# Optimization experiments

Measured on AMD Instinct MI355X. Metric: run time of the kernel, lower is better.

## Reference

```python
import jax, jax.numpy as jnp
import numpy as np

B, S, D, H = 2, 2048, 1024, 16
HD = D // H  # head_dim = 64


def setup_inputs() -> dict:
    key = jax.random.key(0)
    k1, k2, k3 = jax.random.split(key, 3)
    x = jax.random.normal(k1, (B, S, D), dtype=jnp.float32)
    W_attn = jax.random.normal(k2, (3 * D, D), dtype=jnp.float32) * (D ** -0.5)
    W_proj = jax.random.normal(k3, (D, D), dtype=jnp.float32) * (D ** -0.5)
    b_proj = jnp.zeros((D,), dtype=jnp.float32)
    return {"x": x, "W_attn": W_attn, "W_proj": W_proj, "b_proj": b_proj}


def reference(x, W_attn, W_proj, b_proj):
    b, s, d = x.shape
    h, hd = H, d // H
    # fused QKV projection (torch Linear: x @ W^T), then split
    qkv = jnp.einsum('bsd,ed->bse', x, W_attn)  # [B,S,3D]
    q, k, v = jnp.split(qkv, 3, axis=-1)
    # [B,S,D] -> [B,H,S,hd]
    q = q.reshape(b, s, h, hd).transpose(0, 2, 1, 3)
    k = k.reshape(b, s, h, hd).transpose(0, 2, 1, 3)
    v = v.reshape(b, s, h, hd).transpose(0, 2, 1, 3)
    # manual softmax attention (no causal mask in the non-flash branch)
    att = jnp.einsum('bhqd,bhkd->bhqk', q, k) * (1.0 / jnp.sqrt(jnp.float32(hd)))
    att = jax.nn.softmax(att, axis=-1)  # attn_dropout is identity in eval
    y = jnp.einsum('bhqk,bhkd->bhqd', att, v)
    y = y.transpose(0, 2, 1, 3).reshape(b, s, d)
    y = jnp.einsum('bsd,ed->bse', y, W_proj) + b_proj  # resid_dropout identity
    return y, att
```

## Files before the change

### kernel.cpp

```cpp
#include <hip/hip_runtime.h>

typedef _Float16 f16;
typedef f16 f16x4 __attribute__((ext_vector_type(4)));
typedef f16 f16x8 __attribute__((ext_vector_type(8)));
typedef float f32x4 __attribute__((ext_vector_type(4)));
typedef unsigned int u32;
typedef unsigned long long u64;

#define DEV static __device__ __forceinline__

#define S_ 2048
#define D_ 1024

#define S_WAITV(n) asm volatile("s_waitcnt vmcnt(" #n ") lgkmcnt(0)" ::: "memory")

DEV int swz64(int row, int chunk) { return row * 64 + (((chunk ^ row) & 7) << 3); }

DEV void gload16(const void* g, void* l) {
    __builtin_amdgcn_global_load_lds((const __attribute__((address_space(1))) u32*)g,
                                     (__attribute__((address_space(3))) u32*)l, 16, 0, 0);
}
DEV float exp2_fast(float x) { float r; asm("v_exp_f32 %0, %1" : "=v"(r) : "v"(x)); return r; }

__global__ void convert_f16(const float* __restrict__ x, const float* __restrict__ wa,
                            const float* __restrict__ wp,
                            f16* __restrict__ xb, f16* __restrict__ wab, f16* __restrict__ wpb) {
    u32 t = blockIdx.x * blockDim.x + threadIdx.x;
    u32 base = t * 8u;
    const float* src; f16* dst; u32 off;
    if (base < 4194304u)      { src = x;  dst = xb;  off = base; }
    else if (base < 7340032u) { src = wa; dst = wab; off = base - 4194304u; }
    else                      { src = wp; dst = wpb; off = base - 7340032u; }
    float4 a = *(const float4*)(src + off);
    float4 b = *(const float4*)(src + off + 4);
    f16x8 v;
    v[0] = (f16)a.x; v[1] = (f16)a.y; v[2] = (f16)a.z; v[3] = (f16)a.w;
    v[4] = (f16)b.x; v[5] = (f16)b.y; v[6] = (f16)b.z; v[7] = (f16)b.w;
    *(f16x8*)(dst + off) = v;
}

template <int EPI>
__global__ __launch_bounds__(256) void gemm_bt(
    const f16* __restrict__ A, const f16* __restrict__ Bt, int K,
    f16* __restrict__ oQ, f16* __restrict__ oK, f16* __restrict__ oV,
    float* __restrict__ oY, const float* __restrict__ bias) {
    __shared__ f16 smem[8704];
    f16* As = smem;
    f16* Bs = smem + 4096;
    const int tid = threadIdx.x;
    const int lane = tid & 63;
    const int la = lane & 15, lg = lane >> 4;
    const int wv = tid >> 6;
    const int wr = (wv >> 1) << 6, wc = (wv & 1) << 6;
    const int r0 = blockIdx.x << 7, c0 = blockIdx.y << 7;

    const f32x4 VZ = {0.f, 0.f, 0.f, 0.f};
    f32x4 acc[4][4];
#pragma unroll
    for (int m = 0; m < 4; ++m)
#pragma unroll
        for (int n = 0; n < 4; ++n) acc[m][n] = VZ;

    const int srow = tid >> 2, scol = (tid & 3) << 3;
    const f16* Ag = A + (u64)(r0 + srow) * K + scol;
    const f16* Bg = Bt + (u64)(c0 + srow) * K + scol;
    const u64 K64 = (u64)K << 6;
    f16* Al = As + wv * 512;
    f16* Bl = Bs + wv * 512;

    for (int k0 = 0; k0 < K; k0 += 32) {
        __syncthreads();
        gload16(Ag + k0, Al);
        gload16(Ag + K64 + k0, Al + 2048);
        gload16(Bg + k0, Bl);
        gload16(Bg + K64 + k0, Bl + 2048);
        __syncthreads();
        f16x8 af[4], bf[4];
#pragma unroll
        for (int m = 0; m < 4; ++m) af[m] = *(const f16x8*)(As + (wr + m * 16 + la) * 32 + lg * 8);
#pragma unroll
        for (int n = 0; n < 4; ++n) bf[n] = *(const f16x8*)(Bs + (wc + n * 16 + la) * 32 + lg * 8);
#pragma unroll
        for (int m = 0; m < 4; ++m)
#pragma unroll
            for (int n = 0; n < 4; ++n)
                acc[m][n] = __builtin_amdgcn_mfma_f32_16x16x32_f16(af[m], bf[n], acc[m][n], 0, 0, 0);
    }

    if (EPI == 0) {
        if (c0 < 2048) {
#pragma unroll
            for (int n = 0; n < 4; ++n) {
                int col = c0 + wc + n * 16 + la;
#pragma unroll
                for (int m = 0; m < 4; ++m) {
#pragma unroll
                    for (int j = 0; j < 4; ++j) {
                        int row = r0 + wr + m * 16 + lg * 4 + j;
                        int b = row >> 11, s = row & 2047;
                        float val = acc[m][n][j];
                        if (col < 1024) {
                            int h = col >> 6, hd = col & 63;
                            oQ[(((u64)(b * 16 + h)) * 2048 + s) * 64 + hd] = (f16)(val * 0.18033688f);
                        } else {
                            int d = col - 1024, h = d >> 6, hd = d & 63;
                            oK[(((u64)(b * 16 + h)) * 2048 + s) * 64 + hd] = (f16)val;
                        }
                    }
                }
            }
        } else {
            const int hbase = (c0 - 2048) >> 6;
            const int b = r0 >> 11, sb = r0 & 2047;
#pragma unroll
            for (int hh = 0; hh < 2; ++hh) {
                __syncthreads();
                if ((wv & 1) == hh) {
#pragma unroll
                    for (int n = 0; n < 4; ++n) {
                        int hd = n * 16 + la;
#pragma unroll
                        for (int m = 0; m < 4; ++m) {
                            int s = wr + m * 16 + lg * 4;
                            int pos = (s & ~31) | (lg << 3) | (((s >> 4) & 1) << 2);
                            f16x4 pk;
                            pk[0] = (f16)acc[m][n][0]; pk[1] = (f16)acc[m][n][1];
                            pk[2] = (f16)acc[m][n][2]; pk[3] = (f16)acc[m][n][3];
                            *(f16x4*)(smem + hd * 136 + pos) = pk;
                        }
                    }
                }
                __syncthreads();
                {
                    int hd = tid >> 2, qtr = tid & 3;
                    f16* dst = oV + (((u64)(b * 16 + hbase + hh)) * 64 + hd) * 2048 + sb + qtr * 32;
#pragma unroll
                    for (int i = 0; i < 4; ++i)
                        *(f16x8*)(dst + i * 8) = *(const f16x8*)(smem + hd * 136 + qtr * 32 + i * 8);
                }
            }
        }
    } else {
#pragma unroll
        for (int n = 0; n < 4; ++n) {
            int col = c0 + wc + n * 16 + la;
            float bv = bias[col];
#pragma unroll
            for (int m = 0; m < 4; ++m)
#pragma unroll
                for (int j = 0; j < 4; ++j) {
                    int row = r0 + wr + m * 16 + lg * 4 + j;
                    oY[(u64)row * 1024 + col] = acc[m][n][j] + bv;
                }
        }
    }
}

__global__ __launch_bounds__(256) void attn_fused(
    const f16* __restrict__ q, const f16* __restrict__ k, const f16* __restrict__ vt,
    float* __restrict__ att, f16* __restrict__ ya) {
    __shared__ f16 smem[5 * 4096];
    f16* qs = smem + 4 * 4096;

    const int tid = threadIdx.x, lane = tid & 63, wv = tid >> 6;
    const int la = lane & 15, lg = lane >> 4;
    const int qt = blockIdx.x, bh = blockIdx.y;
    const f16* qh = q + (u64)bh * (S_ * 64) + qt * (64 * 64);
    const f16* kh = k + (u64)bh * (S_ * 64);
    const f16* vh = vt + (u64)bh * (S_ * 64);

    const int sr0 = wv * 8 + (lane >> 3);
    const int sr1 = sr0 + 32;
    const int sc0 = (((lane & 7) ^ (sr0 & 7)) << 3);
    const int sc1 = (((lane & 7) ^ (sr1 & 7)) << 3);
    const u64 go0 = (u64)sr0 * 64 + sc0, go1 = (u64)sr1 * 64 + sc1;
    const u64 gv0 = (u64)sr0 * 2048 + sc0, gv1 = (u64)sr1 * 2048 + sc1;

    gload16(qh + go0, qs + wv * 512);
    gload16(qh + go1, qs + 2048 + wv * 512);
    gload16(kh + go0, smem + wv * 512);
    gload16(kh + go1, smem + 2048 + wv * 512);
    gload16(kh + 4096 + go0, smem + 4096 + wv * 512);
    gload16(kh + 4096 + go1, smem + 4096 + 2048 + wv * 512);
    S_WAITV(2);
    __builtin_amdgcn_s_barrier();

    f16x8 qf[2];
    qf[0] = *(const f16x8*)(qs + swz64(wv * 16 + la, lg));
    qf[1] = *(const f16x8*)(qs + swz64(wv * 16 + la, 4 + lg));

    const f32x4 VZ = {0.f, 0.f, 0.f, 0.f};
    float psum = 0.f;

    for (int kt = 0; kt < 32; ++kt) {
        if (kt > 0) {
            if (kt < 31) { S_WAITV(2); } else { S_WAITV(0); }
            __builtin_amdgcn_s_barrier();
        }
        if (kt < 30) {
            const f16* kb = kh + (kt + 2) * 4096;
            f16* dst = smem + ((kt + 2) % 3) * 4096;
            gload16(kb + go0, dst + wv * 512);
            gload16(kb + go1, dst + 2048 + wv * 512);
        }
        const f16* kcur = smem + (kt % 3) * 4096;
        f32x4 sc[4] = {VZ, VZ, VZ, VZ};
#pragma unroll
        for (int ch = 0; ch < 2; ++ch)
#pragma unroll
            for (int n = 0; n < 4; ++n) {
                f16x8 kf = *(const f16x8*)(kcur + swz64(n * 16 + la, ch * 4 + lg));
                sc[n] = __builtin_amdgcn_mfma_f32_16x16x32_f16(kf, qf[ch], sc[n], 0, 0, 0);
            }
#pragma unroll
        for (int n = 0; n < 4; ++n)
#pragma unroll
            for (int j = 0; j < 4; ++j) psum += exp2_fast(sc[n][j]);
    }
    S_WAITV(0);
    __builtin_amdgcn_s_barrier();

    psum += __shfl_xor(psum, 16);
    psum += __shfl_xor(psum, 32);
    const float invl = 1.0f / psum;

    gload16(kh + go0, smem + wv * 512);
    gload16(kh + go1, smem + 2048 + wv * 512);
    gload16(vh + gv0, smem + 2 * 4096 + wv * 512);
    gload16(vh + gv1, smem + 2 * 4096 + 2048 + wv * 512);
    S_WAITV(0);
    __builtin_amdgcn_s_barrier();

    f32x4 accy[4] = {VZ, VZ, VZ, VZ};
    float* ab = att + ((u64)bh * S_ + (u64)qt * 64 + wv * 16 + la) * S_ + (lg << 2);
    for (int kt = 0; kt < 32; ++kt) {
        if (kt > 0) {
            S_WAITV(4);
            __builtin_amdgcn_s_barrier();
        }
        if (kt < 31) {
            const f16* kb = kh + (kt + 1) * 4096;
            const f16* vb = vh + (kt + 1) * 64;
            f16* kd = smem + ((kt + 1) & 1) * 4096;
            f16* vd = smem + (2 + ((kt + 1) & 1)) * 4096;
            gload16(kb + go0, kd + wv * 512);
            gload16(kb + go1, kd + 2048 + wv * 512);
            gload16(vb + gv0, vd + wv * 512);
            gload16(vb + gv1, vd + 2048 + wv * 512);
        }
        const f16* kcur = smem + (kt & 1) * 4096;
        const f16* vcur = smem + (2 + (kt & 1)) * 4096;

        f32x4 sc[4] = {VZ, VZ, VZ, VZ};
#pragma unroll
        for (int ch = 0; ch < 2; ++ch)
#pragma unroll
            for (int n = 0; n < 4; ++n) {
                f16x8 kf = *(const f16x8*)(kcur + swz64(n * 16 + la, ch * 4 + lg));
                sc[n] = __builtin_amdgcn_mfma_f32_16x16x32_f16(kf, qf[ch], sc[n], 0, 0, 0);
            }
        f32x4 pp[4];
#pragma unroll
        for (int n = 0; n < 4; ++n) {
#pragma unroll
            for (int j = 0; j < 4; ++j) pp[n][j] = exp2_fast(sc[n][j]) * invl;
            *(f32x4*)(ab + kt * 64 + n * 16) = pp[n];
        }
        f16x8 pa0, pa1;
#pragma unroll
        for (int j = 0; j < 4; ++j) {
            pa0[j] = (f16)pp[0][j]; pa0[j + 4] = (f16)pp[1][j];
            pa1[j] = (f16)pp[2][j]; pa1[j + 4] = (f16)pp[3][j];
        }
#pragma unroll
        for (int n = 0; n < 4; ++n) {
            f16x8 vf0 = *(const f16x8*)(vcur + swz64(n * 16 + la, lg));
            accy[n] = __builtin_amdgcn_mfma_f32_16x16x32_f16(pa0, vf0, accy[n], 0, 0, 0);
            f16x8 vf1 = *(const f16x8*)(vcur + swz64(n * 16 + la, 4 + lg));
            accy[n] = __builtin_amdgcn_mfma_f32_16x16x32_f16(pa1, vf1, accy[n], 0, 0, 0);
        }
    }

    const int b = bh >> 4, h = bh & 15;
    f16* yb = ya + ((u64)b * S_ + qt * 64 + wv * 16) * D_ + h * 64;
#pragma unroll
    for (int n = 0; n < 4; ++n)
#pragma unroll
        for (int j = 0; j < 4; ++j)
            yb[(u64)(lg * 4 + j) * D_ + n * 16 + la] = (f16)accy[n][j];
}

extern "C" void kernel_launch(void* const* d_in, const int* in_sizes, int n_in,
                              void* d_out, int out_size, void* d_ws, size_t ws_size,
                              hipStream_t stream) {
    const float* x  = (const float*)d_in[0];
    const float* wa = (const float*)d_in[1];
    const float* wp = (const float*)d_in[2];
    const float* bp = (const float*)d_in[3];
    float* outY   = (float*)d_out;
    float* outAtt = outY + 4194304ull;

    char* ws = (char*)d_ws;
    f16* xb  = (f16*)(ws + 0);
    f16* wab = (f16*)(ws + 8388608);
    f16* wpb = (f16*)(ws + 14680064);
    f16* qb  = (f16*)(ws + 16777216);
    f16* kb  = (f16*)(ws + 25165824);
    f16* vtb = (f16*)(ws + 33554432);
    f16* yab = (f16*)(ws + 41943040);

    convert_f16<<<4096, 256, 0, stream>>>(x, wa, wp, xb, wab, wpb);
    gemm_bt<0><<<dim3(32, 24), 256, 0, stream>>>(xb, wab, 1024, qb, kb, vtb, nullptr, nullptr);
    attn_fused<<<dim3(32, 32), 256, 0, stream>>>(qb, kb, vtb, outAtt, yab);
    gemm_bt<1><<<dim3(32, 8), 256, 0, stream>>>(yab, wpb, 1024, nullptr, nullptr, nullptr, outY, bp);
}
```

Baseline: 258.7 us.

## Triple-buffer GEMM LDS tiles with async global-to-LDS prefetch two stages ahead

```diff
diff --git a/kernel.cpp b/kernel.cpp
--- a/kernel.cpp
+++ b/kernel.cpp
@@ -44,9 +44,8 @@
     const f16* __restrict__ A, const f16* __restrict__ Bt, int K,
     f16* __restrict__ oQ, f16* __restrict__ oK, f16* __restrict__ oV,
     float* __restrict__ oY, const float* __restrict__ bias) {
-    __shared__ f16 smem[8704];
-    f16* As = smem;
-    f16* Bs = smem + 4096;
+    __shared__ f16 smem[3][8192];
+    f16* sm = &smem[0][0];
     const int tid = threadIdx.x;
     const int lane = tid & 63;
     const int la = lane & 15, lg = lane >> 4;
@@ -65,16 +64,31 @@
     const f16* Ag = A + (u64)(r0 + srow) * K + scol;
     const f16* Bg = Bt + (u64)(c0 + srow) * K + scol;
     const u64 K64 = (u64)K << 6;
-    f16* Al = As + wv * 512;
-    f16* Bl = Bs + wv * 512;
-
-    for (int k0 = 0; k0 < K; k0 += 32) {
-        __syncthreads();
-        gload16(Ag + k0, Al);
-        gload16(Ag + K64 + k0, Al + 2048);
-        gload16(Bg + k0, Bl);
-        gload16(Bg + K64 + k0, Bl + 2048);
-        __syncthreads();
+
+    const int NT = K >> 5;
+#define STAGE(k0, slot)                                              \
+    do {                                                             \
+        f16* Al = smem[slot] + wv * 512;                             \
+        f16* Bl = smem[slot] + 4096 + wv * 512;                      \
+        gload16(Ag + (k0), Al);                                      \
+        gload16(Ag + K64 + (k0), Al + 2048);                         \
+        gload16(Bg + (k0), Bl);                                      \
+        gload16(Bg + K64 + (k0), Bl + 2048);                         \
+    } while (0)
+
+    STAGE(0, 0);
+    STAGE(32, 1);
+    S_WAITV(4);
+    __builtin_amdgcn_s_barrier();
+
+    for (int t = 0; t < NT; ++t) {
+        if (t > 0) {
+            if (t < NT - 1) { S_WAITV(4); } else { S_WAITV(0); }
+            __builtin_amdgcn_s_barrier();
+        }
+        if (t + 2 < NT) STAGE((t + 2) << 5, (t + 2) % 3);
+        const f16* As = smem[t % 3];
+        const f16* Bs = smem[t % 3] + 4096;
         f16x8 af[4], bf[4];
 #pragma unroll
         for (int m = 0; m < 4; ++m) af[m] = *(const f16x8*)(As + (wr + m * 16 + la) * 32 + lg * 8);
@@ -86,6 +100,7 @@
             for (int n = 0; n < 4; ++n)
                 acc[m][n] = __builtin_amdgcn_mfma_f32_16x16x32_f16(af[m], bf[n], acc[m][n], 0, 0, 0);
     }
+#undef STAGE
 
     if (EPI == 0) {
         if (c0 < 2048) {
@@ -126,7 +141,7 @@
                             f16x4 pk;
                             pk[0] = (f16)acc[m][n][0]; pk[1] = (f16)acc[m][n][1];
                             pk[2] = (f16)acc[m][n][2]; pk[3] = (f16)acc[m][n][3];
-                            *(f16x4*)(smem + hd * 136 + pos) = pk;
+                            *(f16x4*)(sm + hd * 136 + pos) = pk;
                         }
                     }
                 }
@@ -136,7 +151,7 @@
                     f16* dst = oV + (((u64)(b * 16 + hbase + hh)) * 64 + hd) * 2048 + sb + qtr * 32;
 #pragma unroll
                     for (int i = 0; i < 4; ++i)
-                        *(f16x8*)(dst + i * 8) = *(const f16x8*)(smem + hd * 136 + qtr * 32 + i * 8);
+                        *(f16x8*)(dst + i * 8) = *(const f16x8*)(sm + hd * 136 + qtr * 32 + i * 8);
                 }
             }
         }
```

After: 244.7 us. 1.06x faster.
